# Kernel optimization log

Hardware: AMD Instinct MI355X
Metric: run time of the kernel (lower is better)

The kernel has to match this reference:

```python
import jax, jax.numpy as jnp
import numpy as np

V, D, H = 50000, 256, 4
HD = H * D            # concat head dim (TransformerConv concat=True)
HH, O = 256, 256      # invariant_hidden_dim, invariant_out_dim
B, N, E, L, A = 16, 1000, 4000, 64, 128
PAD = 0
SCALE = 1.0 / float(np.sqrt(D))


def emb_lookup(table, idx):
    # nn.Embedding with padding_idx: forward is a plain gather; grad at pad row is zeroed.
    rows = table[idx]
    return jnp.where((idx == PAD)[..., None], jax.lax.stop_gradient(rows), rows)


def transformer_conv(x, edge_index, ea, Wq, bq, Wk, bk, Wv, bv, We, Wskip, bskip):
    # PyG TransformerConv, heads=H, concat=True, root_weight=True, beta=False, dropout=0 (eval)
    n = x.shape[0]
    src, dst = edge_index[0], edge_index[1]
    q = (x @ Wq + bq).reshape(n, H, D)
    e = (ea @ We).reshape(-1, H, D)          # lin_edge (bias=False)
    k = (x @ Wk + bk).reshape(n, H, D)[src] + e
    v = (x @ Wv + bv).reshape(n, H, D)[src] + e
    alpha = (q[dst] * k).sum(-1) * SCALE      # [E,H]
    amax = jax.ops.segment_max(alpha, dst, num_segments=n)
    ex = jnp.exp(alpha - amax[dst])
    denom = jax.ops.segment_sum(ex, dst, num_segments=n)
    w = ex / denom[dst]                       # per-target-node softmax over incoming edges
    agg = jax.ops.segment_sum(v * w[..., None], dst, num_segments=n)
    return agg.reshape(n, HD) + x @ Wskip + bskip  # lin_skip on root


def mixed_embed(tok, node, graph_repr, emb):
    fixed = emb_lookup(emb, tok)
    flex = jnp.take_along_axis(graph_repr, node[..., None], axis=1)
    flex = jnp.where((node == PAD)[..., None], jax.lax.stop_gradient(flex), flex)
    return fixed + flex


def gru_last(xs, W_ih, W_hh, b_ih, b_hh):
    # torch nn.GRU, batch_first, 1 layer; only last hidden state is used
    gx = jnp.einsum('blh,gh->blg', xs, W_ih) + b_ih  # [B,L,3O]

    def step(h, g):
        gh = h @ W_hh.T + b_hh
        xr, xz, xn = jnp.split(g, 3, axis=-1)
        hr, hz, hn = jnp.split(gh, 3, axis=-1)
        r = jax.nn.sigmoid(xr + hr)
        z = jax.nn.sigmoid(xz + hz)
        c = jnp.tanh(xn + r * hn)
        return (1.0 - z) * c + z * h, None

    h0 = jnp.zeros((xs.shape[0], W_hh.shape[1]), xs.dtype)
    h_last, _ = jax.lax.scan(step, h0, jnp.swapaxes(gx, 0, 1))
    return h_last


def setup_inputs() -> dict:
    key = jax.random.key(0)
    ks = jax.random.split(key, 40)
    f = lambda i, shape, s=0.05: jax.random.normal(ks[i], shape, jnp.float32) * s
    ri = lambda i, shape, hi: jax.random.randint(ks[i], shape, 0, hi)
    return {
        'node_tokens': ri(0, (B, N), V),
        'edge_tokens': ri(1, (B, E), V),
        'edge_index': ri(2, (B, 2, E), N),
        'inv_token': ri(3, (B, L), V),
        'inv_node': ri(4, (B, L), N),
        'aa_token': ri(5, (B, A), V),
        'aa_node': ri(6, (B, A), N),
        'action_mask': jnp.ones((B, A), jnp.float32),
        'emb': f(7, (V, D), 0.02),
        'Wq': f(8, (D, HD)), 'bq': f(9, (HD,)),
        'Wk': f(10, (D, HD)), 'bk': f(11, (HD,)),
        'Wv': f(12, (D, HD)), 'bv': f(13, (HD,)),
        'We': f(14, (D, HD)),
        'Wskip': f(15, (D, HD)), 'bskip': f(16, (HD,)),
        'W1': f(17, (HD, D)), 'b1': f(18, (D,)),
        'Wp': f(19, (D, HH)), 'bp': f(20, (HH,)),
        'W_ih': f(21, (3 * O, HH)), 'W_hh': f(22, (3 * O, O)),
        'b_ih': f(23, (3 * O,)), 'b_hh': f(24, (3 * O,)),
        'Wab': f(25, (D, 1)), 'bab': f(26, (1,)),
        'Wap': f(27, (D, O)), 'bap': f(28, (O,)),
    }


def reference(node_tokens, edge_tokens, edge_index, inv_token, inv_node, aa_token, aa_node,
              action_mask, emb, Wq, bq, Wk, bk, Wv, bv, We, Wskip, bskip, W1, b1,
              Wp, bp, W_ih, W_hh, b_ih, b_hh, Wab, bab, Wap, bap):
    x = emb_lookup(emb, node_tokens)    # [B,N,D]
    ea = emb_lookup(emb, edge_tokens)   # [B,E,D]
    conv = jax.vmap(lambda xx, ei, ee: transformer_conv(
        xx, ei, ee, Wq, bq, Wk, bk, Wv, bv, We, Wskip, bskip))
    h = jax.nn.relu(conv(x, edge_index, ea))            # [B,N,HD]
    graph_repr = jax.nn.relu(h @ W1 + b1)               # [B,N,D]
    inv_h = jax.nn.relu(mixed_embed(inv_token, inv_node, graph_repr, emb) @ Wp + bp)
    inv = gru_last(inv_h, W_ih, W_hh, b_ih, b_hh)       # [B,O]
    aa_emb = mixed_embed(aa_token, aa_node, graph_repr, emb)  # [B,A,D]
    scores = jnp.einsum('bao,bo->ba', aa_emb @ Wap + bap, inv) + (aa_emb @ Wab + bab)[..., 0]
    inf_mask = jnp.maximum(jnp.log(action_mask), jnp.float32(np.finfo(np.float32).min))
    return scores + inf_mask
```

## Files before the change

kernel.cpp:

```cpp
#include <hip/hip_runtime.h>
#include <hip/hip_bf16.h>
#include <float.h>
#include <math.h>

typedef __hip_bfloat16 bf16;

#define B_ 16
#define N_ 1000
#define E_ 4000
#define L_ 64
#define A_ 128
#define D_ 256
#define H_ 4
#define HD_ 1024
#define SCALE_ 0.0625f

typedef __attribute__((ext_vector_type(8))) short short8;
typedef __attribute__((ext_vector_type(4))) float f32x4;

union U4S8 { uint4 u; short8 s; };

__device__ __forceinline__ unsigned short f2bf(float f) {
    bf16 h = __float2bfloat16(f);
    return *reinterpret_cast<unsigned short*>(&h);
}
__device__ __forceinline__ unsigned pack2(float a, float b) {
    return (unsigned)f2bf(a) | ((unsigned)f2bf(b) << 16);
}
__device__ __forceinline__ unsigned short rne1(float a) {
    unsigned ua = __float_as_uint(a);
    ua += 0x7fff + ((ua >> 16) & 1);
    return (unsigned short)(ua >> 16);
}
__device__ __forceinline__ float bflo(unsigned u) { return __uint_as_float(u << 16); }
__device__ __forceinline__ float bfhi(unsigned u) { return __uint_as_float(u & 0xffff0000u); }

#define LOG2E 1.4426950408889634f
__device__ __forceinline__ float fsigm(float x) {
    return __builtin_amdgcn_rcpf(1.f + __builtin_amdgcn_exp2f(-LOG2E * x));
}
__device__ __forceinline__ float ftanh(float x) {
    return 1.f - 2.f * __builtin_amdgcn_rcpf(1.f + __builtin_amdgcn_exp2f(2.f * LOG2E * x));
}

typedef const __attribute__((address_space(1))) unsigned int* gas_t;
typedef __attribute__((address_space(3))) unsigned int* las_t;
__device__ __forceinline__ void gld16(const void* g, void* l) {
    __builtin_amdgcn_global_load_lds((gas_t)g, (las_t)l, 16, 0, 0);
}

__global__ void convemb_kernel(const float* __restrict__ src, bf16* __restrict__ dst, long n4)
{
    long i = (long)blockIdx.x * 256 + threadIdx.x;
    if (i >= n4) return;
    float4 v = *(const float4*)(src + i * 4);
    *(uint2*)(dst + i * 4) = make_uint2(pack2(v.x, v.y), pack2(v.z, v.w));
}

__global__ void pack_all_kernel(const float* __restrict__ Wq, const float* __restrict__ Wk,
                                const float* __restrict__ Wv, const float* __restrict__ Wskip,
                                const float* __restrict__ We, const float* __restrict__ W1,
                                const float* __restrict__ Wp, const float* __restrict__ W_ih,
                                const float* __restrict__ Wap, const float* __restrict__ W_hh,
                                const float* __restrict__ bq, const float* __restrict__ bk,
                                const float* __restrict__ bv, const float* __restrict__ bskip,
                                unsigned* __restrict__ qkvsP, unsigned* __restrict__ WeP,
                                unsigned* __restrict__ W1P, unsigned* __restrict__ WpP,
                                unsigned* __restrict__ WihP, unsigned* __restrict__ WapP,
                                unsigned* __restrict__ WeTP,
                                short8* __restrict__ WhhP, float* __restrict__ bias4096)
{
    int i = blockIdx.x * 256 + threadIdx.x;
    if (i < 524288) {
        int k2 = i >> 12, n = i & 4095;
        const float* s = (n < 1024) ? Wq : (n < 2048) ? Wk : (n < 3072) ? Wv : Wskip;
        int col = n & 1023;
        qkvsP[i] = pack2(s[(long)(2 * k2) * 1024 + col], s[(long)(2 * k2 + 1) * 1024 + col]);
        return;
    }
    i -= 524288;
    if (i < 131072) {
        int k2 = i >> 10, n = i & 1023;
        WeP[i] = pack2(We[(long)(2 * k2) * 1024 + n], We[(long)(2 * k2 + 1) * 1024 + n]);
        return;
    }
    i -= 131072;
    if (i < 131072) {
        int k2 = i >> 8, n = i & 255;
        W1P[i] = pack2(W1[(long)(2 * k2) * 256 + n], W1[(long)(2 * k2 + 1) * 256 + n]);
        return;
    }
    i -= 131072;
    if (i < 32768) {
        int k2 = i >> 8, n = i & 255;
        WpP[i] = pack2(Wp[(long)(2 * k2) * 256 + n], Wp[(long)(2 * k2 + 1) * 256 + n]);
        return;
    }
    i -= 32768;
    if (i < 98304) {
        int k2 = i / 768, n = i % 768;
        WihP[i] = pack2(W_ih[(long)n * 256 + 2 * k2], W_ih[(long)n * 256 + 2 * k2 + 1]);
        return;
    }
    i -= 98304;
    if (i < 32768) {
        int k2 = i >> 8, n = i & 255;
        WapP[i] = pack2(Wap[(long)(2 * k2) * 256 + n], Wap[(long)(2 * k2 + 1) * 256 + n]);
        return;
    }
    i -= 32768;
    if (i < 131072) {
        int k2 = i >> 10, n = i & 1023;
        int d = n & 255, hb = n & ~255;
        WeTP[i] = pack2(We[(long)d * 1024 + hb + 2 * k2],
                        We[(long)d * 1024 + hb + 2 * k2 + 1]);
        return;
    }
    i -= 131072;
    if (i < 24576) {
        int lane = i & 63, tk = (i >> 6) & 7, tile = i >> 9;
        int n = tile * 16 + (lane & 15);
        const float* wp = W_hh + (long)n * 256 + tk * 32 + (lane >> 4) * 8;
        float4 w0 = *(const float4*)wp;
        float4 w1 = *(const float4*)(wp + 4);
        U4S8 u;
        u.u = make_uint4(pack2(w0.x, w0.y), pack2(w0.z, w0.w),
                         pack2(w1.x, w1.y), pack2(w1.z, w1.w));
        WhhP[i] = u.s;
        return;
    }
    i -= 24576;
    if (i < 4096) {
        int q = i >> 10, c = i & 1023;
        bias4096[i] = ((q == 0) ? bq : (q == 1) ? bk : (q == 2) ? bv : bskip)[c];
    }
}
#define PACK_ALL_TOT (524288 + 131072 + 131072 + 32768 + 98304 + 32768 + 131072 + 24576 + 4096)

#define TM 128
#define TN 128
#define TK 32
#define BSTR 132

template <typename CT>
__global__ __launch_bounds__(256)
void pgemm_kernel(const bf16* __restrict__ A, const int* __restrict__ arows,
                  const unsigned* __restrict__ Bp, const float* __restrict__ bias,
                  CT* __restrict__ C, int M, int K, int Nc, int relu_out,
                  long astride, int aoff, int colbase, int hslice, int addC, int outT)
{
    __shared__ short    As[TM * TK];
    __shared__ unsigned Bs[(TK / 2) * BSTR];

    const int tid  = threadIdx.x;
    const int lane = tid & 63;
    const int wave = tid >> 6;
    const int wm = wave >> 1, wn = wave & 1;
    const int quad = lane >> 4, c16 = lane & 15;
    const long row0 = (long)blockIdx.y * TM;
    const int  col0 = colbase + blockIdx.x * TN;
    const int  aoff2 = aoff + (hslice ? (col0 & ~255) : 0);

    const int r0 = wave * 32 + (lane >> 2);
    const int cseg = (lane & 3) * 8;
    long gr0 = row0 + r0;      if (gr0 > M - 1) gr0 = M - 1;
    long gr1 = row0 + r0 + 16; if (gr1 > M - 1) gr1 = M - 1;
    long ar0 = arows ? (long)arows[gr0] : gr0;
    long ar1 = arows ? (long)arows[gr1] : gr1;
    const short* Ag0 = (const short*)A + ar0 * astride + aoff2 + cseg;
    const short* Ag1 = (const short*)A + ar1 * astride + aoff2 + cseg;
    short* Ld0 = &As[wave * 1024];
    short* Ld1 = &As[wave * 1024 + 512];

    const int sn2 = tid & 63;
    const int skk = wave * 4;

    f32x4 acc[4][4];
    #pragma unroll
    for (int i = 0; i < 4; ++i)
        #pragma unroll
        for (int j = 0; j < 4; ++j)
            acc[i][j] = (f32x4){0.f, 0.f, 0.f, 0.f};

    for (int k0 = 0; k0 < K; k0 += TK) {
        gld16(Ag0 + k0, Ld0);
        gld16(Ag1 + k0, Ld1);
        #pragma unroll
        for (int i = 0; i < 4; ++i) {
            int kk2 = skk + i;
            *(uint2*)&Bs[kk2 * BSTR + sn2 * 2] =
                *(const uint2*)&Bp[(long)(k0 / 2 + kk2) * Nc + col0 + sn2 * 2];
        }
        __syncthreads();

        short8 af[4];
        U4S8   bfr[4];
        #pragma unroll
        for (int mi = 0; mi < 4; ++mi) {
            int m = wm * 64 + mi * 16 + c16;
            af[mi] = *(const short8*)&As[m * 32 + quad * 8];
        }
        #pragma unroll
        for (int ni = 0; ni < 4; ++ni) {
            int n = wn * 64 + ni * 16 + c16;
            uint4 u;
            u.x = Bs[(quad * 4 + 0) * BSTR + n];
            u.y = Bs[(quad * 4 + 1) * BSTR + n];
            u.z = Bs[(quad * 4 + 2) * BSTR + n];
            u.w = Bs[(quad * 4 + 3) * BSTR + n];
            bfr[ni].u = u;
        }
        #pragma unroll
        for (int mi = 0; mi < 4; ++mi)
            #pragma unroll
            for (int ni = 0; ni < 4; ++ni)
                acc[mi][ni] = __builtin_amdgcn_mfma_f32_16x16x32_bf16(
                    af[mi], bfr[ni].s, acc[mi][ni], 0, 0, 0);
        __syncthreads();
    }

    #pragma unroll
    for (int ni = 0; ni < 4; ++ni) {
        int col = col0 + wn * 64 + ni * 16 + c16;
        float bv = bias ? bias[col] : 0.f;
        #pragma unroll
        for (int mi = 0; mi < 4; ++mi) {
            long row = row0 + wm * 64 + mi * 16 + quad * 4;
            #pragma unroll
            for (int r = 0; r < 4; ++r) {
                if (row + r >= M) continue;
                float v = acc[mi][ni][r] + bv;
                if (addC) v += (float)C[(row + r) * Nc + col];
                if (relu_out) v = fmaxf(v, 0.f);
                if (outT) {
                    long rr = row + r;
                    int t = (int)(rr & 63), b = (int)(rr >> 6);
                    C[((long)t * Nc + col) * 16 + b] = (CT)v;
                } else {
                    C[(row + r) * Nc + col] = (CT)v;
                }
            }
        }
    }
}

__global__ void zero_int_kernel(int* __restrict__ p, int n)
{
    int i = blockIdx.x * 256 + threadIdx.x;
    if (i < n) p[i] = 0;
}

__global__ void count_kernel(const int* __restrict__ edge_index, int b0,
                             int* __restrict__ cnt, int cE)
{
    int i = blockIdx.x * 256 + threadIdx.x;
    if (i >= cE) return;
    int bl = i / E_, ei = i % E_;
    int dst = edge_index[(long)(b0 + bl) * 2 * E_ + E_ + ei];
    atomicAdd(&cnt[bl * N_ + dst], 1);
}

__global__ __launch_bounds__(1024)
void scan_kernel(const int* __restrict__ cnt, int* __restrict__ row_start,
                 int* __restrict__ cursor)
{
    int bl = blockIdx.x;
    int tid = threadIdx.x;
    __shared__ int s[1024];
    int v = (tid < N_) ? cnt[bl * N_ + tid] : 0;
    s[tid] = v;
    __syncthreads();
    for (int off = 1; off < 1024; off <<= 1) {
        int t = (tid >= off) ? s[tid - off] : 0;
        __syncthreads();
        s[tid] += t;
        __syncthreads();
    }
    if (tid < N_) {
        int excl = s[tid] - v;
        row_start[bl * N_ + tid] = excl;
        cursor[bl * N_ + tid] = excl;
    }
}

__global__ void scatter_kernel(const int* __restrict__ edge_index, int b0,
                               int* __restrict__ cursor, int* __restrict__ elist, int cE)
{
    int i = blockIdx.x * 256 + threadIdx.x;
    if (i >= cE) return;
    int bl = i / E_, ei = i % E_;
    int dst = edge_index[(long)(b0 + bl) * 2 * E_ + E_ + ei];
    int pos = atomicAdd(&cursor[bl * N_ + dst], 1);
    elist[bl * E_ + pos] = ei;
}

__device__ __forceinline__ float d2(unsigned a, unsigned b)
{
    return bflo(a) * bflo(b) + bfhi(a) * bfhi(b);
}

__global__ void attn_kernel(const bf16* __restrict__ qkvs, const bf16* __restrict__ qWb,
                            const bf16* __restrict__ embh,
                            const int* __restrict__ edge_tokens, const int* __restrict__ edge_index,
                            const int* __restrict__ row_start, const int* __restrict__ cnt,
                            const int* __restrict__ elist, int b0,
                            bf16* __restrict__ aggb, bf16* __restrict__ xsumb)
{
    int base = blockIdx.x;
    int bl = base / N_;
    int tid = threadIdx.x;
    int l = tid & 63;
    int j0 = tid * 4;
    int jx = l * 4;

    uint2 qq = *(const uint2*)(qkvs + (long)base * 4096 + j0);
    uint2 ww = *(const uint2*)(qWb + (long)base * 1024 + j0);

    int start = row_start[base];
    int deg = cnt[base];
    const int* el = elist + (long)bl * E_;
    const int* srcp = edge_index + (long)(b0 + bl) * 2 * E_;
    const int* tokp = edge_tokens + (long)(b0 + bl) * E_;

    float denom = 0.f;
    float v0 = 0.f, v1 = 0.f, v2 = 0.f, v3 = 0.f;
    float x0 = 0.f, x1 = 0.f, x2 = 0.f, x3 = 0.f;

    uint2 kk = make_uint2(0, 0), vv = make_uint2(0, 0), xx = make_uint2(0, 0);
    if (deg > 0) {
        int e0 = el[start];
        int s0 = srcp[e0], t0 = tokp[e0];
        const bf16* srow = qkvs + (long)(bl * N_ + s0) * 4096;
        kk = *(const uint2*)(srow + 1024 + j0);
        vv = *(const uint2*)(srow + 2048 + j0);
        xx = *(const uint2*)(embh + (long)t0 * 256 + jx);
    }

    for (int t = 0; t < deg; ++t) {
        uint2 ck = kk, cv = vv, cx = xx;
        if (t + 1 < deg) {
            int ne = el[start + t + 1];
            int ns = srcp[ne], nt = tokp[ne];
            const bf16* srow = qkvs + (long)(bl * N_ + ns) * 4096;
            kk = *(const uint2*)(srow + 1024 + j0);
            vv = *(const uint2*)(srow + 2048 + j0);
            xx = *(const uint2*)(embh + (long)nt * 256 + jx);
        }

        float s = d2(qq.x, ck.x) + d2(qq.y, ck.y) + d2(ww.x, cx.x) + d2(ww.y, cx.y);
        s += __shfl_xor(s, 32);
        s += __shfl_xor(s, 16);
        s += __shfl_xor(s, 8);
        s += __shfl_xor(s, 4);
        s += __shfl_xor(s, 2);
        s += __shfl_xor(s, 1);
        float ex = __builtin_amdgcn_exp2f(s * (SCALE_ * LOG2E));

        denom += ex;
        v0 += ex * bflo(cv.x); v1 += ex * bfhi(cv.x);
        v2 += ex * bflo(cv.y); v3 += ex * bfhi(cv.y);
        x0 += ex * bflo(cx.x); x1 += ex * bfhi(cx.x);
        x2 += ex * bflo(cx.y); x3 += ex * bfhi(cx.y);
    }

    float invd = (deg > 0) ? 1.f / denom : 0.f;
    uint2 sk = *(const uint2*)(qkvs + (long)base * 4096 + 3072 + j0);
    unsigned o0 = pack2(bflo(sk.x) + v0 * invd, bfhi(sk.x) + v1 * invd);
    unsigned o1 = pack2(bflo(sk.y) + v2 * invd, bfhi(sk.y) + v3 * invd);
    *(uint2*)(aggb + (long)base * HD_ + j0) = make_uint2(o0, o1);
    *(uint2*)(xsumb + (long)base * HD_ + j0) =
        make_uint2(pack2(x0 * invd, x1 * invd), pack2(x2 * invd, x3 * invd));
}

__global__ void mixed2_kernel(const bf16* __restrict__ embh,
                              const int* __restrict__ inv_token, const int* __restrict__ inv_node,
                              const int* __restrict__ aa_token, const int* __restrict__ aa_node,
                              const bf16* __restrict__ graph_repr,
                              bf16* __restrict__ mixed_inv, bf16* __restrict__ aa_emb)
{
    int r = blockIdx.x;
    int d = threadIdx.x;
    if (r < B_ * L_) {
        int b = r / L_;
        float v = (float)embh[(long)inv_token[r] * D_ + d] +
                  (float)graph_repr[((long)b * N_ + inv_node[r]) * D_ + d];
        mixed_inv[(long)r * D_ + d] = __float2bfloat16(v);
    } else {
        int r2 = r - B_ * L_;
        int b = r2 / A_;
        float v = (float)embh[(long)aa_token[r2] * D_ + d] +
                  (float)graph_repr[((long)b * N_ + aa_node[r2]) * D_ + d];
        aa_emb[(long)r2 * D_ + d] = __float2bfloat16(v);
    }
}

__global__ __launch_bounds__(1024)
void gru_kernel(const bf16* __restrict__ gxT, const short8* __restrict__ WhhP,
                const float* __restrict__ b_hh, float* __restrict__ inv_out)
{
    __shared__ short hB[2][16 * 264];

    const int tid = threadIdx.x;
    const int lane = tid & 63;
    const int wave = tid >> 6;
    const int quad = lane >> 4, c16 = lane & 15;
    const int n0 = wave * 16 + c16;
    const int bb = blockIdx.x * 4 + quad;

    for (int i = tid; i < 2 * 16 * 264; i += 1024) ((short*)hB)[i] = 0;

    short8 wfr[8], wfz[8], wfn[8];
    #pragma unroll
    for (int tk = 0; tk < 8; ++tk) {
        wfr[tk] = WhhP[((0 * 16 + wave) * 8 + tk) * 64 + lane];
        wfz[tk] = WhhP[((1 * 16 + wave) * 8 + tk) * 64 + lane];
        wfn[tk] = WhhP[((2 * 16 + wave) * 8 + tk) * 64 + lane];
    }
    float bhr = b_hh[0 * 256 + n0];
    float bhz = b_hh[1 * 256 + n0];
    float bhn = b_hh[2 * 256 + n0];

    float myh = 0.f;

    const unsigned short* g_r = (const unsigned short*)gxT + (long)n0 * 16 + bb;
    const unsigned short* g_z = g_r + 256 * 16;
    const unsigned short* g_n = g_r + 512 * 16;

    unsigned short pr = g_r[0], pz = g_z[0], pn = g_n[0];

    __syncthreads();

    int p = 0;
    for (int t = 0; t < L_; ++t) {
        float xr = __uint_as_float((unsigned)pr << 16);
        float xz = __uint_as_float((unsigned)pz << 16);
        float xn = __uint_as_float((unsigned)pn << 16);
        long noff = (long)((t + 1 < L_) ? t + 1 : t) * 12288;
        pr = g_r[noff]; pz = g_z[noff]; pn = g_n[noff];

        f32x4 ar = (f32x4){bhr, bhr, bhr, bhr};
        f32x4 az = (f32x4){bhz, bhz, bhz, bhz};
        f32x4 an = (f32x4){bhn, bhn, bhn, bhn};
        const short* hp = &hB[p][0];
        #pragma unroll
        for (int tk = 0; tk < 8; ++tk) {
            short8 a = *(const short8*)&hp[c16 * 264 + tk * 32 + quad * 8];
            ar = __builtin_amdgcn_mfma_f32_16x16x32_bf16(a, wfr[tk], ar, 0, 0, 0);
            az = __builtin_amdgcn_mfma_f32_16x16x32_bf16(a, wfz[tk], az, 0, 0, 0);
            an = __builtin_amdgcn_mfma_f32_16x16x32_bf16(a, wfn[tk], an, 0, 0, 0);
        }

        float rr = fsigm(xr + ar[0]);
        float zz = fsigm(xz + az[0]);
        float cc = ftanh(xn + rr * an[0]);
        myh = (1.f - zz) * cc + zz * myh;
        hB[p ^ 1][(quad * 4) * 264 + n0] = (short)rne1(myh);
        p ^= 1;
        __syncthreads();
    }

    inv_out[(long)bb * 256 + n0] = myh;
}

__global__ void uprep_kernel(const float* __restrict__ Wap, const float* __restrict__ Wab,
                             const float* __restrict__ bap, const float* __restrict__ bab,
                             const float* __restrict__ inv, float* __restrict__ u,
                             float* __restrict__ s0)
{
    int b = blockIdx.x, d = threadIdx.x;
    __shared__ float iv[256];
    iv[d] = inv[(long)b * 256 + d];
    __syncthreads();
    float s = Wab[d];
    const float* wr = Wap + (long)d * 256;
    #pragma unroll 8
    for (int o = 0; o < 256; ++o) s += wr[o] * iv[o];
    u[(long)b * 256 + d] = s;
    if (d == 0) {
        float t = bab[0];
        for (int o = 0; o < 256; ++o) t += bap[o] * iv[o];
        s0[b] = t;
    }
}

__global__ void score_kernel(const bf16* __restrict__ aa_emb, const float* __restrict__ u,
                             const float* __restrict__ s0, const float* __restrict__ mask,
                             float* __restrict__ out)
{
    int r = blockIdx.x * 4 + (threadIdx.x >> 6);
    int l = threadIdx.x & 63;
    int b = r / A_;
    float s = 0.f;
    for (int d = l; d < D_; d += 64)
        s += (float)aa_emb[(long)r * D_ + d] * u[(long)b * D_ + d];
    #pragma unroll
    for (int off = 32; off; off >>= 1) s += __shfl_down(s, off);
    if (l == 0) {
        float lm = logf(mask[r]);
        const float MN = -3.4028234663852886e38f;
        if (!(lm >= MN)) lm = MN;
        out[r] = s + s0[b] + lm;
    }
}

static inline size_t align256(size_t x) { return (x + 255) & ~(size_t)255; }

template <typename CT>
static void launch_pgemm(const bf16* A, const int* arows, const unsigned* Bp,
                         const float* bias, CT* C, int M, int K, int Nc, int relu,
                         long astride, int aoff, int colbase, int hslice, int addC,
                         int outT, int ncols, hipStream_t s)
{
    dim3 grid(ncols / TN, (M + TM - 1) / TM);
    pgemm_kernel<CT><<<grid, 256, 0, s>>>(A, arows, Bp, bias, C, M, K, Nc, relu,
                                          astride, aoff, colbase, hslice, addC, outT);
}

extern "C" void kernel_launch(void* const* d_in, const int* in_sizes, int n_in,
                              void* d_out, int out_size, void* d_ws, size_t ws_size,
                              hipStream_t stream)
{
    const int* node_tokens = (const int*)d_in[0];
    const int* edge_tokens = (const int*)d_in[1];
    const int* edge_index  = (const int*)d_in[2];
    const int* inv_token   = (const int*)d_in[3];
    const int* inv_node    = (const int*)d_in[4];
    const int* aa_token    = (const int*)d_in[5];
    const int* aa_node     = (const int*)d_in[6];
    const float* action_mask = (const float*)d_in[7];
    const float* emb   = (const float*)d_in[8];
    const float* Wq    = (const float*)d_in[9];
    const float* bq    = (const float*)d_in[10];
    const float* Wk    = (const float*)d_in[11];
    const float* bk    = (const float*)d_in[12];
    const float* Wv    = (const float*)d_in[13];
    const float* bv    = (const float*)d_in[14];
    const float* We    = (const float*)d_in[15];
    const float* Wskip = (const float*)d_in[16];
    const float* bskip = (const float*)d_in[17];
    const float* W1    = (const float*)d_in[18];
    const float* b1    = (const float*)d_in[19];
    const float* Wp    = (const float*)d_in[20];
    const float* bp    = (const float*)d_in[21];
    const float* W_ih  = (const float*)d_in[22];
    const float* W_hh  = (const float*)d_in[23];
    const float* b_ih  = (const float*)d_in[24];
    const float* b_hh  = (const float*)d_in[25];
    const float* Wab   = (const float*)d_in[26];
    const float* bab   = (const float*)d_in[27];
    const float* Wap   = (const float*)d_in[28];
    const float* bap   = (const float*)d_in[29];
    (void)in_sizes; (void)n_in; (void)out_size;

    char* base = (char*)d_ws;
    size_t off = 0;
    auto alloc = [&](size_t bytes) -> char* {
        char* p = base + off;
        off = align256(off + bytes);
        return p;
    };

    const long VD = 50000L * 256;
    bf16*  embh       = (bf16*)alloc(VD * 2);
    bf16*  graph_repr = (bf16*)alloc((size_t)B_ * N_ * D_ * 2);
    bf16*  mixed_inv  = (bf16*)alloc((size_t)B_ * L_ * D_ * 2);
    bf16*  inv_h      = (bf16*)alloc((size_t)B_ * L_ * D_ * 2);
    bf16*  gxT        = (bf16*)alloc((size_t)B_ * L_ * 768 * 2);
    float* inv_out    = (float*)alloc((size_t)B_ * 256 * 4);
    bf16*  aa_emb     = (bf16*)alloc((size_t)B_ * A_ * D_ * 2);
    float* ubuf       = (float*)alloc((size_t)B_ * 256 * 4);
    float* s0buf      = (float*)alloc((size_t)B_ * 4);
    unsigned* qkvsP   = (unsigned*)alloc((size_t)128 * 4096 * 4);
    unsigned* WeP     = (unsigned*)alloc((size_t)128 * 1024 * 4);
    unsigned* W1P     = (unsigned*)alloc((size_t)512 * 256 * 4);
    unsigned* WpP     = (unsigned*)alloc((size_t)128 * 256 * 4);
    unsigned* WihP    = (unsigned*)alloc((size_t)128 * 768 * 4);
    unsigned* WapP    = (unsigned*)alloc((size_t)128 * 256 * 4);
    unsigned* WeTP    = (unsigned*)alloc((size_t)128 * 1024 * 4);
    short8* WhhP      = (short8*)alloc((size_t)24576 * 16);
    float* bias4096   = (float*)alloc(4096 * 4);
    size_t persist = off;

    int c = 16;
    while (c > 1) {
        size_t cN = (size_t)c * N_, cEs = (size_t)c * E_;
        size_t chunk = align256(cN * 4096 * 2)
                     + align256(cN * HD_ * 2)
                     + align256(cN * HD_ * 2)
                     + align256(cN * HD_ * 2)
                     + 3 * align256(cN * 4)
                     + align256(cEs * 4);
        if (persist + chunk <= ws_size) break;
        c >>= 1;
    }
    int cN = c * N_, cE = c * E_;

    bf16*  qkvs  = (bf16*)alloc((size_t)cN * 4096 * 2);
    bf16*  qWb   = (bf16*)alloc((size_t)cN * HD_ * 2);
    bf16*  aggb  = (bf16*)alloc((size_t)cN * HD_ * 2);
    bf16*  xsumb = (bf16*)alloc((size_t)cN * HD_ * 2);
    int*   cnt   = (int*)alloc((size_t)cN * 4);
    int*   rstart= (int*)alloc((size_t)cN * 4);
    int*   cursor= (int*)alloc((size_t)cN * 4);
    int*   elist = (int*)alloc((size_t)cE * 4);

    convemb_kernel<<<(int)((VD / 4 + 255) / 256), 256, 0, stream>>>(emb, embh, VD / 4);
    pack_all_kernel<<<(PACK_ALL_TOT + 255) / 256, 256, 0, stream>>>(
        Wq, Wk, Wv, Wskip, We, W1, Wp, W_ih, Wap, W_hh, bq, bk, bv, bskip,
        qkvsP, WeP, W1P, WpP, WihP, WapP, WeTP, WhhP, bias4096);

    for (int b0 = 0; b0 < B_; b0 += c) {
        zero_int_kernel<<<(cN + 255) / 256, 256, 0, stream>>>(cnt, cN);
        count_kernel<<<(cE + 255) / 256, 256, 0, stream>>>(edge_index, b0, cnt, cE);
        scan_kernel<<<c, 1024, 0, stream>>>(cnt, rstart, cursor);
        scatter_kernel<<<(cE + 255) / 256, 256, 0, stream>>>(edge_index, b0, cursor,
                                                             elist, cE);
        launch_pgemm<bf16>(embh, node_tokens + (long)b0 * N_, qkvsP, bias4096, qkvs,
                           cN, D_, 4096, 0, 256, 0, 0, 0, 0, 0, 4096, stream);
        launch_pgemm<bf16>(qkvs, nullptr, WeTP, nullptr, qWb,
                           cN, 256, 1024, 0, 4096, 0, 0, 1, 0, 0, 1024, stream);
        attn_kernel<<<cN, 256, 0, stream>>>(qkvs, qWb, embh, edge_tokens, edge_index,
                                            rstart, cnt, elist, b0, aggb, xsumb);
        launch_pgemm<bf16>(xsumb, nullptr, WeP, nullptr, aggb,
                           cN, 256, 1024, 1, 1024, 0, 0, 1, 1, 0, 1024, stream);
        launch_pgemm<bf16>(aggb, nullptr, W1P, b1,
                           graph_repr + (long)b0 * N_ * D_,
                           cN, HD_, D_, 1, 1024, 0, 0, 0, 0, 0, 256, stream);
    }

    mixed2_kernel<<<B_ * L_ + B_ * A_, 256, 0, stream>>>(embh, inv_token, inv_node,
                                                         aa_token, aa_node, graph_repr,
                                                         mixed_inv, aa_emb);
    launch_pgemm<bf16>(mixed_inv, nullptr, WpP, bp, inv_h,
                       B_ * L_, D_, 256, 1, 256, 0, 0, 0, 0, 0, 256, stream);
    launch_pgemm<bf16>(inv_h, nullptr, WihP, b_ih, gxT,
                       B_ * L_, 256, 768, 0, 256, 0, 0, 0, 0, 1, 768, stream);
    gru_kernel<<<4, 1024, 0, stream>>>(gxT, WhhP, b_hh, inv_out);

    uprep_kernel<<<B_, 256, 0, stream>>>(Wap, Wab, bap, bab, inv_out, ubuf, s0buf);
    score_kernel<<<(B_ * A_) / 4, 256, 0, stream>>>(aa_emb, ubuf, s0buf,
                                                    action_mask, (float*)d_out);
}
```

Measured before the change: 798.3 us.

## Fuse CSR build into one kernel, unroll attention edges by two, deepen GRU prefetch

Replaces the four zero/count/scan/scatter launches per chunk with one block-per-graph kernel that counts, scans and scatters in shared memory. The attention loop now handles two edges per iteration, issuing both gathers together to expose more memory-level parallelism, in place of a one-ahead prefetch. The GRU input-gate loads are prefetched two steps ahead, and the unused Wap packing is dropped. The fused CSR kernel runs one 1024-thread block per graph, which limits parallelism, and edge order within each destination list may change.

```diff
diff --git a/kernel.cpp b/kernel.cpp
--- a/kernel.cpp
+++ b/kernel.cpp
@@ -66,8 +66,7 @@
                                 const float* __restrict__ bv, const float* __restrict__ bskip,
                                 unsigned* __restrict__ qkvsP, unsigned* __restrict__ WeP,
                                 unsigned* __restrict__ W1P, unsigned* __restrict__ WpP,
-                                unsigned* __restrict__ WihP, unsigned* __restrict__ WapP,
-                                unsigned* __restrict__ WeTP,
+                                unsigned* __restrict__ WihP, unsigned* __restrict__ WeTP,
                                 short8* __restrict__ WhhP, float* __restrict__ bias4096)
 {
     int i = blockIdx.x * 256 + threadIdx.x;
@@ -103,12 +102,6 @@
         return;
     }
     i -= 98304;
-    if (i < 32768) {
-        int k2 = i >> 8, n = i & 255;
-        WapP[i] = pack2(Wap[(long)(2 * k2) * 256 + n], Wap[(long)(2 * k2 + 1) * 256 + n]);
-        return;
-    }
-    i -= 32768;
     if (i < 131072) {
         int k2 = i >> 10, n = i & 1023;
         int d = n & 255, hb = n & ~255;
@@ -135,7 +128,7 @@
         bias4096[i] = ((q == 0) ? bq : (q == 1) ? bk : (q == 2) ? bv : bskip)[c];
     }
 }
-#define PACK_ALL_TOT (524288 + 131072 + 131072 + 32768 + 98304 + 32768 + 131072 + 24576 + 4096)
+#define PACK_ALL_TOT (524288 + 131072 + 131072 + 32768 + 98304 + 131072 + 24576 + 4096)
 
 #define TM 128
 #define TN 128
@@ -244,54 +237,49 @@
     }
 }
 
-__global__ void zero_int_kernel(int* __restrict__ p, int n)
-{
-    int i = blockIdx.x * 256 + threadIdx.x;
-    if (i < n) p[i] = 0;
-}
-
-__global__ void count_kernel(const int* __restrict__ edge_index, int b0,
-                             int* __restrict__ cnt, int cE)
-{
-    int i = blockIdx.x * 256 + threadIdx.x;
-    if (i >= cE) return;
-    int bl = i / E_, ei = i % E_;
-    int dst = edge_index[(long)(b0 + bl) * 2 * E_ + E_ + ei];
-    atomicAdd(&cnt[bl * N_ + dst], 1);
-}
-
 __global__ __launch_bounds__(1024)
-void scan_kernel(const int* __restrict__ cnt, int* __restrict__ row_start,
-                 int* __restrict__ cursor)
+void csr_kernel(const int* __restrict__ edge_index, int b0,
+                int* __restrict__ row_start, int* __restrict__ cntg,
+                int* __restrict__ elist)
 {
     int bl = blockIdx.x;
     int tid = threadIdx.x;
-    __shared__ int s[1024];
-    int v = (tid < N_) ? cnt[bl * N_ + tid] : 0;
-    s[tid] = v;
+    __shared__ int scnt[1024];
+    __shared__ int sscan[1024];
+
+    scnt[tid] = 0;
+    __syncthreads();
+
+    const int* dstp = edge_index + (long)(b0 + bl) * 2 * E_ + E_;
+    #pragma unroll
+    for (int e = tid; e < E_; e += 1024)
+        atomicAdd(&scnt[dstp[e]], 1);
+    __syncthreads();
+
+    int v = scnt[tid];
+    sscan[tid] = v;
     __syncthreads();
     for (int off = 1; off < 1024; off <<= 1) {
-        int t = (tid >= off) ? s[tid - off] : 0;
+        int t = (tid >= off) ? sscan[tid - off] : 0;
         __syncthreads();
-        s[tid] += t;
+        sscan[tid] += t;
         __syncthreads();
     }
+    int excl = sscan[tid] - v;
     if (tid < N_) {
-        int excl = s[tid] - v;
         row_start[bl * N_ + tid] = excl;
-        cursor[bl * N_ + tid] = excl;
-    }
-}
-
-__global__ void scatter_kernel(const int* __restrict__ edge_index, int b0,
-                               int* __restrict__ cursor, int* __restrict__ elist, int cE)
-{
-    int i = blockIdx.x * 256 + threadIdx.x;
-    if (i >= cE) return;
-    int bl = i / E_, ei = i % E_;
-    int dst = edge_index[(long)(b0 + bl) * 2 * E_ + E_ + ei];
-    int pos = atomicAdd(&cursor[bl * N_ + dst], 1);
-    elist[bl * E_ + pos] = ei;
+        cntg[bl * N_ + tid] = v;
+    }
+    __syncthreads();
+    scnt[tid] = excl;
+    __syncthreads();
+
+    int* el = elist + (long)bl * E_;
+    #pragma unroll
+    for (int e = tid; e < E_; e += 1024) {
+        int pos = atomicAdd(&scnt[dstp[e]], 1);
+        el[pos] = e;
+    }
 }
 
 __device__ __forceinline__ float d2(unsigned a, unsigned b)
@@ -326,41 +314,62 @@
     float v0 = 0.f, v1 = 0.f, v2 = 0.f, v3 = 0.f;
     float x0 = 0.f, x1 = 0.f, x2 = 0.f, x3 = 0.f;
 
-    uint2 kk = make_uint2(0, 0), vv = make_uint2(0, 0), xx = make_uint2(0, 0);
-    if (deg > 0) {
-        int e0 = el[start];
-        int s0 = srcp[e0], t0 = tokp[e0];
-        const bf16* srow = qkvs + (long)(bl * N_ + s0) * 4096;
-        kk = *(const uint2*)(srow + 1024 + j0);
-        vv = *(const uint2*)(srow + 2048 + j0);
-        xx = *(const uint2*)(embh + (long)t0 * 256 + jx);
-    }
-
-    for (int t = 0; t < deg; ++t) {
-        uint2 ck = kk, cv = vv, cx = xx;
-        if (t + 1 < deg) {
-            int ne = el[start + t + 1];
-            int ns = srcp[ne], nt = tokp[ne];
-            const bf16* srow = qkvs + (long)(bl * N_ + ns) * 4096;
-            kk = *(const uint2*)(srow + 1024 + j0);
-            vv = *(const uint2*)(srow + 2048 + j0);
-            xx = *(const uint2*)(embh + (long)nt * 256 + jx);
-        }
-
-        float s = d2(qq.x, ck.x) + d2(qq.y, ck.y) + d2(ww.x, cx.x) + d2(ww.y, cx.y);
-        s += __shfl_xor(s, 32);
-        s += __shfl_xor(s, 16);
-        s += __shfl_xor(s, 8);
-        s += __shfl_xor(s, 4);
-        s += __shfl_xor(s, 2);
-        s += __shfl_xor(s, 1);
-        float ex = __builtin_amdgcn_exp2f(s * (SCALE_ * LOG2E));
-
-        denom += ex;
-        v0 += ex * bflo(cv.x); v1 += ex * bfhi(cv.x);
-        v2 += ex * bflo(cv.y); v3 += ex * bfhi(cv.y);
-        x0 += ex * bflo(cx.x); x1 += ex * bfhi(cx.x);
-        x2 += ex * bflo(cx.y); x3 += ex * bfhi(cx.y);
+    int t = 0;
+    while (t + 1 < deg) {
+        int ea = el[start + t], eb2 = el[start + t + 1];
+        int sa = srcp[ea], sb = srcp[eb2];
+        int ta = tokp[ea], tb = tokp[eb2];
+        const bf16* ra = qkvs + (long)(bl * N_ + sa) * 4096;
+        const bf16* rb = qkvs + (long)(bl * N_ + sb) * 4096;
+        uint2 ka = *(const uint2*)(ra + 1024 + j0);
+        uint2 kb = *(const uint2*)(rb + 1024 + j0);
+        uint2 va = *(const uint2*)(ra + 2048 + j0);
+        uint2 vb = *(const uint2*)(rb + 2048 + j0);
+        uint2 xa = *(const uint2*)(embh + (long)ta * 256 + jx);
+        uint2 xb = *(const uint2*)(embh + (long)tb * 256 + jx);
+
+        float s1 = d2(qq.x, ka.x) + d2(qq.y, ka.y) + d2(ww.x, xa.x) + d2(ww.y, xa.y);
+        float s2 = d2(qq.x, kb.x) + d2(qq.y, kb.y) + d2(ww.x, xb.x) + d2(ww.y, xb.y);
+        s1 += __shfl_xor(s1, 32);  s2 += __shfl_xor(s2, 32);
+        s1 += __shfl_xor(s1, 16);  s2 += __shfl_xor(s2, 16);
+        s1 += __shfl_xor(s1, 8);   s2 += __shfl_xor(s2, 8);
+        s1 += __shfl_xor(s1, 4);   s2 += __shfl_xor(s2, 4);
+        s1 += __shfl_xor(s1, 2);   s2 += __shfl_xor(s2, 2);
+        s1 += __shfl_xor(s1, 1);   s2 += __shfl_xor(s2, 1);
+        float exa = __builtin_amdgcn_exp2f(s1 * (SCALE_ * LOG2E));
+        float exb = __builtin_amdgcn_exp2f(s2 * (SCALE_ * LOG2E));
+
+        denom += exa + exb;
+        v0 += exa * bflo(va.x) + exb * bflo(vb.x);
+        v1 += exa * bfhi(va.x) + exb * bfhi(vb.x);
+        v2 += exa * bflo(va.y) + exb * bflo(vb.y);
+        v3 += exa * bfhi(va.y) + exb * bfhi(vb.y);
+        x0 += exa * bflo(xa.x) + exb * bflo(xb.x);
+        x1 += exa * bfhi(xa.x) + exb * bfhi(xb.x);
+        x2 += exa * bflo(xa.y) + exb * bflo(xb.y);
+        x3 += exa * bfhi(xa.y) + exb * bfhi(xb.y);
+        t += 2;
+    }
+    if (t < deg) {
+        int ea = el[start + t];
+        int sa = srcp[ea], ta = tokp[ea];
+        const bf16* ra = qkvs + (long)(bl * N_ + sa) * 4096;
+        uint2 ka = *(const uint2*)(ra + 1024 + j0);
+        uint2 va = *(const uint2*)(ra + 2048 + j0);
+        uint2 xa = *(const uint2*)(embh + (long)ta * 256 + jx);
+        float s1 = d2(qq.x, ka.x) + d2(qq.y, ka.y) + d2(ww.x, xa.x) + d2(ww.y, xa.y);
+        s1 += __shfl_xor(s1, 32);
+        s1 += __shfl_xor(s1, 16);
+        s1 += __shfl_xor(s1, 8);
+        s1 += __shfl_xor(s1, 4);
+        s1 += __shfl_xor(s1, 2);
+        s1 += __shfl_xor(s1, 1);
+        float exa = __builtin_amdgcn_exp2f(s1 * (SCALE_ * LOG2E));
+        denom += exa;
+        v0 += exa * bflo(va.x); v1 += exa * bfhi(va.x);
+        v2 += exa * bflo(va.y); v3 += exa * bfhi(va.y);
+        x0 += exa * bflo(xa.x); x1 += exa * bfhi(xa.x);
+        x2 += exa * bflo(xa.y); x3 += exa * bfhi(xa.y);
     }
 
     float invd = (deg > 0) ? 1.f / denom : 0.f;
@@ -426,17 +435,19 @@
     const unsigned short* g_z = g_r + 256 * 16;
     const unsigned short* g_n = g_r + 512 * 16;
 
-    unsigned short pr = g_r[0], pz = g_z[0], pn = g_n[0];
+    unsigned short pr0 = g_r[0], pz0 = g_z[0], pn0 = g_n[0];
+    unsigned short pr1 = g_r[12288], pz1 = g_z[12288], pn1 = g_n[12288];
 
     __syncthreads();
 
     int p = 0;
     for (int t = 0; t < L_; ++t) {
-        float xr = __uint_as_float((unsigned)pr << 16);
-        float xz = __uint_as_float((unsigned)pz << 16);
-        float xn = __uint_as_float((unsigned)pn << 16);
-        long noff = (long)((t + 1 < L_) ? t + 1 : t) * 12288;
-        pr = g_r[noff]; pz = g_z[noff]; pn = g_n[noff];
+        float xr = __uint_as_float((unsigned)pr0 << 16);
+        float xz = __uint_as_float((unsigned)pz0 << 16);
+        float xn = __uint_as_float((unsigned)pn0 << 16);
+        pr0 = pr1; pz0 = pz1; pn0 = pn1;
+        long noff = (long)((t + 2 < L_) ? t + 2 : L_ - 1) * 12288;
+        pr1 = g_r[noff]; pz1 = g_z[noff]; pn1 = g_n[noff];
 
         f32x4 ar = (f32x4){bhr, bhr, bhr, bhr};
         f32x4 az = (f32x4){bhz, bhz, bhz, bhz};
@@ -575,7 +586,6 @@
     unsigned* W1P     = (unsigned*)alloc((size_t)512 * 256 * 4);
     unsigned* WpP     = (unsigned*)alloc((size_t)128 * 256 * 4);
     unsigned* WihP    = (unsigned*)alloc((size_t)128 * 768 * 4);
-    unsigned* WapP    = (unsigned*)alloc((size_t)128 * 256 * 4);
     unsigned* WeTP    = (unsigned*)alloc((size_t)128 * 1024 * 4);
     short8* WhhP      = (short8*)alloc((size_t)24576 * 16);
     float* bias4096   = (float*)alloc(4096 * 4);
@@ -588,7 +598,7 @@
                      + align256(cN * HD_ * 2)
                      + align256(cN * HD_ * 2)
                      + align256(cN * HD_ * 2)
-                     + 3 * align256(cN * 4)
+                     + 2 * align256(cN * 4)
                      + align256(cEs * 4);
         if (persist + chunk <= ws_size) break;
         c >>= 1;
@@ -601,20 +611,15 @@
     bf16*  xsumb = (bf16*)alloc((size_t)cN * HD_ * 2);
     int*   cnt   = (int*)alloc((size_t)cN * 4);
     int*   rstart= (int*)alloc((size_t)cN * 4);
-    int*   cursor= (int*)alloc((size_t)cN * 4);
     int*   elist = (int*)alloc((size_t)cE * 4);
 
     convemb_kernel<<<(int)((VD / 4 + 255) / 256), 256, 0, stream>>>(emb, embh, VD / 4);
     pack_all_kernel<<<(PACK_ALL_TOT + 255) / 256, 256, 0, stream>>>(
         Wq, Wk, Wv, Wskip, We, W1, Wp, W_ih, Wap, W_hh, bq, bk, bv, bskip,
-        qkvsP, WeP, W1P, WpP, WihP, WapP, WeTP, WhhP, bias4096);
+        qkvsP, WeP, W1P, WpP, WihP, WeTP, WhhP, bias4096);
 
     for (int b0 = 0; b0 < B_; b0 += c) {
-        zero_int_kernel<<<(cN + 255) / 256, 256, 0, stream>>>(cnt, cN);
-        count_kernel<<<(cE + 255) / 256, 256, 0, stream>>>(edge_index, b0, cnt, cE);
-        scan_kernel<<<c, 1024, 0, stream>>>(cnt, rstart, cursor);
-        scatter_kernel<<<(cE + 255) / 256, 256, 0, stream>>>(edge_index, b0, cursor,
-                                                             elist, cE);
+        csr_kernel<<<c, 1024, 0, stream>>>(edge_index, b0, rstart, cnt, elist);
         launch_pgemm<bf16>(embh, node_tokens + (long)b0 * N_, qkvsP, bias4096, qkvs,
                            cN, D_, 4096, 0, 256, 0, 0, 0, 0, 0, 4096, stream);
         launch_pgemm<bf16>(qkvs, nullptr, WeTP, nullptr, qWb,
```

Measured after the change: 859.5 us. 1.08x slower.
